# Kernel tuning notes

Hardware: AMD Instinct MI355X
Metric: run time of the kernel (lower is better)

Reference implementation:

```python
import jax, jax.numpy as jnp
import numpy as np
import math

B, N, CS, CZ, CH, H, PQK, PV = 1, 1024, 384, 128, 16, 12, 4, 8
INF, EPS = 1e5, 1e-8


def quat_to_rot(q):
    w, x, y, z = q[..., 0], q[..., 1], q[..., 2], q[..., 3]
    r = jnp.stack([
        1 - 2 * (y * y + z * z), 2 * (x * y - w * z), 2 * (x * z + w * y),
        2 * (x * y + w * z), 1 - 2 * (x * x + z * z), 2 * (y * z - w * x),
        2 * (x * z - w * y), 2 * (y * z + w * x), 1 - 2 * (x * x + y * y),
    ], axis=-1)
    return r.reshape(q.shape[:-1] + (3, 3))


def setup_inputs() -> dict:
    key = jax.random.key(0)
    ks = jax.random.split(key, 12)
    sc = 0.02
    s = jax.random.normal(ks[0], (B, N, CS), jnp.float32)
    z = jax.random.normal(ks[1], (B, N, N, CZ), jnp.float32)
    quat = jax.random.normal(ks[2], (B, N, 4), jnp.float32)
    rot = quat_to_rot(quat / jnp.linalg.norm(quat, axis=-1, keepdims=True))
    trans = jax.random.normal(ks[3], (B, N, 3), jnp.float32)
    mask = jnp.ones((B, N), jnp.float32)
    wq = jax.random.normal(ks[4], (CS, H * CH), jnp.float32) * sc
    bq = jnp.zeros((H * CH,), jnp.float32)
    wkv = jax.random.normal(ks[5], (CS, 2 * H * CH), jnp.float32) * sc
    bkv = jnp.zeros((2 * H * CH,), jnp.float32)
    wqp = jax.random.normal(ks[6], (CS, H * PQK * 3), jnp.float32) * sc
    bqp = jnp.zeros((H * PQK * 3,), jnp.float32)
    wkvp = jax.random.normal(ks[7], (CS, H * (PQK + PV) * 3), jnp.float32) * sc
    bkvp = jnp.zeros((H * (PQK + PV) * 3,), jnp.float32)
    wb = jax.random.normal(ks[8], (CZ, H), jnp.float32) * sc
    bb = jnp.zeros((H,), jnp.float32)
    head_w = jax.random.normal(ks[9], (H,), jnp.float32) * 0.1 + 0.5413  # softplus^-1(1)
    dcat = H * (CZ + CH + PV * 4)
    wout = jax.random.normal(ks[10], (dcat, CS), jnp.float32) * sc
    bout = jnp.zeros((CS,), jnp.float32)
    return dict(s=s, z=z, rot=rot, trans=trans, mask=mask, wq=wq, bq=bq,
                wkv=wkv, bkv=bkv, wqp=wqp, bqp=bqp, wkvp=wkvp, bkvp=bkvp,
                wb=wb, bb=bb, head_w=head_w, wout=wout, bout=bout)


def reference(s, z, rot, trans, mask, wq, bq, wkv, bkv, wqp, bqp, wkvp, bkvp,
              wb, bb, head_w, wout, bout):
    # scalar q/k/v: [B,N,H,CH]
    q = (s @ wq + bq).reshape(B, N, H, CH)
    kv = (s @ wkv + bkv).reshape(B, N, H, 2 * CH)
    k, v = kv[..., :CH], kv[..., CH:]

    def make_pts(raw, P):
        # raw layout: [x-coords | y-coords | z-coords], each of width H*P
        pts = jnp.swapaxes(raw.reshape(B, N, 3, H * P), -1, -2)  # [B,N,H*P,3]
        pts = jnp.einsum('bnxy,bnpy->bnpx', rot, pts) + trans[:, :, None, :]
        return pts.reshape(B, N, H, P, 3)

    q_pts = make_pts(s @ wqp + bqp, PQK)                 # [B,N,H,PQK,3] global frame
    kv_pts = make_pts(s @ wkvp + bkvp, PQK + PV)
    k_pts, v_pts = kv_pts[..., :PQK, :], kv_pts[..., PQK:, :]

    # scalar attention + pair bias: [B,H,N,N]
    a = jnp.einsum('bihc,bjhc->bhij', q, k) * math.sqrt(1.0 / (3 * CH))
    bias = z @ wb + bb                                    # [B,N,N,H]
    a = a + math.sqrt(1.0 / 3) * jnp.transpose(bias, (0, 3, 1, 2))

    # point attention via ||q-k||^2 = |q|^2 + |k|^2 - 2 q.k (summed over pts & xyz)
    hw = jax.nn.softplus(head_w) * math.sqrt(1.0 / (3 * (PQK * 9.0 / 2)))  # [H]
    qn = jnp.sum(q_pts ** 2, axis=(-1, -2))               # [B,N,H]
    kn = jnp.sum(k_pts ** 2, axis=(-1, -2))
    cross = jnp.einsum('bihpx,bjhpx->bhij', q_pts, k_pts)
    sqd = (jnp.transpose(qn, (0, 2, 1))[..., None]
           + jnp.transpose(kn, (0, 2, 1))[:, :, None, :]
           - 2.0 * cross)                                 # [B,H,N,N]
    a = a - 0.5 * hw[None, :, None, None] * sqd

    sqm = INF * (mask[:, :, None] * mask[:, None, :] - 1.0)  # [B,N,N]
    a = jax.nn.softmax(a + sqm[:, None], axis=-1)

    # outputs
    o = jnp.einsum('bhij,bjhc->bihc', a, v).reshape(B, N, H * CH)
    o_pt = jnp.einsum('bhij,bjhpx->bihpx', a, v_pts)      # [B,N,H,PV,3] global
    o_pt = jnp.einsum('bnyx,bnhpy->bnhpx', rot, o_pt - trans[:, :, None, None, :])  # invert_apply
    o_pt_norm = jnp.sqrt(jnp.sum(o_pt ** 2, axis=-1) + EPS).reshape(B, N, H * PV)
    o_pt3 = o_pt.reshape(B, N, H * PV, 3)
    o_pair = jnp.einsum('bhij,bijc->bihc', a, z).reshape(B, N, H * CZ)

    cat = jnp.concatenate(
        [o, o_pt3[..., 0], o_pt3[..., 1], o_pt3[..., 2], o_pt_norm, o_pair], axis=-1)
    return cat @ wout + bout
```

## Files before the change

### kernel.cpp

```cpp
#include <hip/hip_runtime.h>
#include <hip/hip_bf16.h>
#include <math.h>

#define NN   1024
#define CS   384
#define CZ   128
#define HH   12
#define HCH  192
#define QPR  144
#define DCAT 2112
#define PROJW 1152
#define INF_ 100000.0f

#define SC_QK 0.14433756729740643f
#define SC_B  0.5773502691896258f
#define SC_PT 0.13608276348795434f

__device__ __forceinline__ float dot4(float4 a, float4 b) {
  return a.x * b.x + a.y * b.y + a.z * b.z + a.w * b.w;
}
__device__ __forceinline__ float bf2f(unsigned short u) {
  unsigned int v = ((unsigned int)u) << 16;
  float f; __builtin_memcpy(&f, &v, 4); return f;
}
__device__ __forceinline__ unsigned short f2bf(float f) {
  __hip_bfloat16 h = __float2bfloat16(f);
  unsigned short u; __builtin_memcpy(&u, &h, 2); return u;
}

__global__ void prep(const float* __restrict__ wb, const float* __restrict__ head_w,
                     float* __restrict__ wb_t, float* __restrict__ hw)
{
  int t = threadIdx.x;
  for (int idx = t; idx < CZ * HH; idx += 256) {
    int c = idx % CZ, h = idx / CZ;
    wb_t[h * CZ + c] = wb[c * HH + h];
  }
  if (t < HH) {
    float x = head_w[t];
    float sp = (x > 20.f) ? x : log1pf(__expf(x));
    hw[t] = sp * SC_PT;
  }
}

__global__ __launch_bounds__(256) void proj_all(
    const float* __restrict__ s,
    const float* __restrict__ wq, const float* __restrict__ bq,
    const float* __restrict__ wkv, const float* __restrict__ bkv,
    const float* __restrict__ wqp, const float* __restrict__ bqp,
    const float* __restrict__ wkvp, const float* __restrict__ bkvp,
    float* __restrict__ proj)
{
  __shared__ float s_lds[8 * CS];
  const int n0 = blockIdx.x * 8;
  for (int idx = threadIdx.x; idx < 8 * CS; idx += 256)
    s_lds[idx] = s[(size_t)(n0 + idx / CS) * CS + (idx % CS)];
  __syncthreads();

  const int gc = blockIdx.y * 128 + (threadIdx.x & 31) * 4;
  const int rg = threadIdx.x >> 5;
  const float* wp; const float* bp; int OUT, lc;
  if (gc < 192)      { wp = wq;   bp = bq;   OUT = 192; lc = gc; }
  else if (gc < 576) { wp = wkv;  bp = bkv;  OUT = 384; lc = gc - 192; }
  else if (gc < 720) { wp = wqp;  bp = bqp;  OUT = 144; lc = gc - 576; }
  else               { wp = wkvp; bp = bkvp; OUT = 432; lc = gc - 720; }

  float a0 = 0.f, a1 = 0.f, a2 = 0.f, a3 = 0.f;
  const float* srow = &s_lds[rg * CS];
#pragma unroll 4
  for (int kk = 0; kk < CS; kk++) {
    float sv = srow[kk];
    float4 w4 = *reinterpret_cast<const float4*>(&wp[(size_t)kk * OUT + lc]);
    a0 += sv * w4.x; a1 += sv * w4.y; a2 += sv * w4.z; a3 += sv * w4.w;
  }
  float* o = proj + (size_t)(n0 + rg) * PROJW + gc;
  o[0] = a0 + bp[lc]; o[1] = a1 + bp[lc + 1];
  o[2] = a2 + bp[lc + 2]; o[3] = a3 + bp[lc + 3];
}

__global__ __launch_bounds__(256) void ipa_transform(
    const float* __restrict__ proj, const float* __restrict__ rot,
    const float* __restrict__ trans,
    float* __restrict__ kc, float* __restrict__ vc,
    float* __restrict__ q_pts, float* __restrict__ kpc,
    float* __restrict__ vpc, float* __restrict__ qn, float* __restrict__ knc)
{
  const int n = blockIdx.x, tid = threadIdx.x;
  const float* pr = proj + (size_t)n * PROJW;
  __shared__ float R[9], T[3], sq_q[48], sq_k[48];
  if (tid < 9) R[tid] = rot[n * 9 + tid];
  if (tid < 3) T[tid] = trans[n * 3 + tid];
  __syncthreads();
  if (tid < HCH) {
    int h = tid >> 4, c = tid & 15;
    kc[(size_t)(h * 16 + c) * NN + n] = pr[192 + h * 32 + c];
    vc[(size_t)(h * 16 + c) * NN + n] = pr[192 + h * 32 + 16 + c];
  }
  if (tid < 48) {
    float r0 = pr[576 + tid], r1 = pr[576 + 48 + tid], r2 = pr[576 + 96 + tid];
    float x = R[0] * r0 + R[1] * r1 + R[2] * r2 + T[0];
    float y = R[3] * r0 + R[4] * r1 + R[5] * r2 + T[1];
    float z = R[6] * r0 + R[7] * r1 + R[8] * r2 + T[2];
    q_pts[(size_t)n * QPR + tid * 3 + 0] = x;
    q_pts[(size_t)n * QPR + tid * 3 + 1] = y;
    q_pts[(size_t)n * QPR + tid * 3 + 2] = z;
    sq_q[tid] = x * x + y * y + z * z;
  }
  if (tid >= 64 && tid < 208) {
    int t = tid - 64;
    float r0 = pr[720 + t], r1 = pr[720 + 144 + t], r2 = pr[720 + 288 + t];
    float x = R[0] * r0 + R[1] * r1 + R[2] * r2 + T[0];
    float y = R[3] * r0 + R[4] * r1 + R[5] * r2 + T[1];
    float z = R[6] * r0 + R[7] * r1 + R[8] * r2 + T[2];
    int h = t / 12, pp = t % 12;
    if (pp < 4) {
      int d = pp * 3;
      kpc[(size_t)(h * 12 + d + 0) * NN + n] = x;
      kpc[(size_t)(h * 12 + d + 1) * NN + n] = y;
      kpc[(size_t)(h * 12 + d + 2) * NN + n] = z;
      sq_k[h * 4 + pp] = x * x + y * y + z * z;
    } else {
      int d = (pp - 4) * 3;
      vpc[(size_t)(h * 24 + d + 0) * NN + n] = x;
      vpc[(size_t)(h * 24 + d + 1) * NN + n] = y;
      vpc[(size_t)(h * 24 + d + 2) * NN + n] = z;
    }
  }
  __syncthreads();
  if (tid < HH) {
    float a = 0.f, b = 0.f;
#pragma unroll
    for (int p = 0; p < 4; p++) { a += sq_q[tid * 4 + p]; b += sq_k[tid * 4 + p]; }
    qn[n * HH + tid] = a;
    knc[(size_t)tid * NN + n] = b;
  }
}

__global__ __launch_bounds__(256) void bias_pass(
    const float* __restrict__ z, const float* __restrict__ wb_t,
    __hip_bfloat16* __restrict__ B)
{
  __shared__ float wb_s[HH * CZ];
  __shared__ float bias_s[HH * 128];
  const int i = blockIdx.y;
  const int jb = blockIdx.x * 128;
  const int tid = threadIdx.x;
  const int jl = tid >> 2, csub = tid & 3;

  for (int e = tid; e < HH * CZ; e += 256) wb_s[e] = wb_t[e];
  __syncthreads();

  float bd0[HH], bd1[HH];
#pragma unroll
  for (int h = 0; h < HH; h++) { bd0[h] = 0.f; bd1[h] = 0.f; }

  const float* zb = z + ((size_t)i * NN + jb + jl) * CZ + csub * 4;
#pragma unroll
  for (int k8 = 0; k8 < 8; k8++) {
    float4 zq0 = *reinterpret_cast<const float4*>(&zb[k8 * 16]);
    float4 zq1 = *reinterpret_cast<const float4*>(&zb[(size_t)64 * CZ + k8 * 16]);
    const int c = csub * 4 + k8 * 16;
#pragma unroll
    for (int h = 0; h < HH; h++) {
      float4 wv = *reinterpret_cast<const float4*>(&wb_s[h * CZ + c]);
      bd0[h] += dot4(zq0, wv);
      bd1[h] += dot4(zq1, wv);
    }
  }
#pragma unroll
  for (int h = 0; h < HH; h++) {
    bd0[h] += __shfl_xor(bd0[h], 1); bd0[h] += __shfl_xor(bd0[h], 2);
    bd1[h] += __shfl_xor(bd1[h], 1); bd1[h] += __shfl_xor(bd1[h], 2);
  }
  if (csub == 0) {
#pragma unroll
    for (int h = 0; h < HH; h++) {
      bias_s[h * 128 + jl] = bd0[h];
      bias_s[h * 128 + 64 + jl] = bd1[h];
    }
  }
  __syncthreads();
  for (int e = tid; e < HH * 128; e += 256) {
    int h = e >> 7, j2 = e & 127;
    B[((size_t)i * HH + h) * NN + jb + j2] = __float2bfloat16(bias_s[e]);
  }
}

__global__ __launch_bounds__(256) void ipa_attn(
    const float* __restrict__ kc, const float* __restrict__ kpc,
    const float* __restrict__ knc, const float* __restrict__ vc,
    const float* __restrict__ vpc, const float* __restrict__ proj,
    const float* __restrict__ q_pts, const float* __restrict__ qn,
    const float* __restrict__ bb, const float* __restrict__ hw,
    const float* __restrict__ mask,
    __hip_bfloat16* __restrict__ A, float* __restrict__ cat,
    float* __restrict__ optb)
{
  const int h = blockIdx.y;
  const int i = blockIdx.x * 4 + (threadIdx.x >> 6);
  const int lane = threadIdx.x & 63;

  const float* qb = proj + (size_t)i * PROJW + h * 16;
  const float4 q0 = *reinterpret_cast<const float4*>(qb);
  const float4 q1 = *reinterpret_cast<const float4*>(qb + 4);
  const float4 q2 = *reinterpret_cast<const float4*>(qb + 8);
  const float4 q3 = *reinterpret_cast<const float4*>(qb + 12);
  const float* pb = q_pts + (size_t)i * QPR + h * 12;
  const float4 p0 = *reinterpret_cast<const float4*>(pb);
  const float4 p1 = *reinterpret_cast<const float4*>(pb + 4);
  const float4 p2 = *reinterpret_cast<const float4*>(pb + 8);
  const float qnv = qn[i * HH + h];
  const float bbv = bb[h];
  const float hwv = hw[h];
  const float mi = mask[i];

  const float* kch  = kc  + (size_t)h * 16 * NN;
  const float* kpch = kpc + (size_t)h * 12 * NN;
  const float* knch = knc + (size_t)h * NN;
  const float* vch  = vc  + (size_t)h * 16 * NN;
  const float* vpch = vpc + (size_t)h * 24 * NN;
  __hip_bfloat16* Arow = A + ((size_t)i * HH + h) * NN;

  float4 av[4];
#pragma unroll
  for (int t = 0; t < 4; t++) {
    const int j = t * 256 + lane * 4;
    float4 d = {0, 0, 0, 0};
#pragma unroll
    for (int c = 0; c < 16; c++) {
      const float qc = (c < 4 ? (&q0.x)[c] : c < 8 ? (&q1.x)[c - 4]
                       : c < 12 ? (&q2.x)[c - 8] : (&q3.x)[c - 12]);
      float4 kv = *reinterpret_cast<const float4*>(&kch[(size_t)c * NN + j]);
      d.x += qc * kv.x; d.y += qc * kv.y; d.z += qc * kv.z; d.w += qc * kv.w;
    }
    float4 cr = {0, 0, 0, 0};
#pragma unroll
    for (int dd = 0; dd < 12; dd++) {
      const float pc = (dd < 4 ? (&p0.x)[dd] : dd < 8 ? (&p1.x)[dd - 4]
                        : (&p2.x)[dd - 8]);
      float4 kv = *reinterpret_cast<const float4*>(&kpch[(size_t)dd * NN + j]);
      cr.x += pc * kv.x; cr.y += pc * kv.y; cr.z += pc * kv.z; cr.w += pc * kv.w;
    }
    float4 kn4 = *reinterpret_cast<const float4*>(&knch[j]);
    ushort4 bu = *reinterpret_cast<const ushort4*>(&Arow[j]);
    float4 m4 = *reinterpret_cast<const float4*>(&mask[j]);
    av[t].x = SC_QK * d.x + SC_B * (bf2f(bu.x) + bbv)
              - 0.5f * hwv * (qnv + kn4.x - 2.f * cr.x) + INF_ * (mi * m4.x - 1.f);
    av[t].y = SC_QK * d.y + SC_B * (bf2f(bu.y) + bbv)
              - 0.5f * hwv * (qnv + kn4.y - 2.f * cr.y) + INF_ * (mi * m4.y - 1.f);
    av[t].z = SC_QK * d.z + SC_B * (bf2f(bu.z) + bbv)
              - 0.5f * hwv * (qnv + kn4.z - 2.f * cr.z) + INF_ * (mi * m4.z - 1.f);
    av[t].w = SC_QK * d.w + SC_B * (bf2f(bu.w) + bbv)
              - 0.5f * hwv * (qnv + kn4.w - 2.f * cr.w) + INF_ * (mi * m4.w - 1.f);
  }

  float m = av[0].x;
#pragma unroll
  for (int t = 0; t < 4; t++) {
    m = fmaxf(m, av[t].x); m = fmaxf(m, av[t].y);
    m = fmaxf(m, av[t].z); m = fmaxf(m, av[t].w);
  }
  for (int off = 32; off; off >>= 1) m = fmaxf(m, __shfl_xor(m, off));
  float ssum = 0.f;
#pragma unroll
  for (int t = 0; t < 4; t++) {
    av[t].x = __expf(av[t].x - m); ssum += av[t].x;
    av[t].y = __expf(av[t].y - m); ssum += av[t].y;
    av[t].z = __expf(av[t].z - m); ssum += av[t].z;
    av[t].w = __expf(av[t].w - m); ssum += av[t].w;
  }
  for (int off = 32; off; off >>= 1) ssum += __shfl_xor(ssum, off);
  const float inv = 1.f / ssum;
#pragma unroll
  for (int t = 0; t < 4; t++) {
    const int j = t * 256 + lane * 4;
    av[t].x *= inv; av[t].y *= inv; av[t].z *= inv; av[t].w *= inv;
    ushort4 st;
    st.x = f2bf(av[t].x); st.y = f2bf(av[t].y);
    st.z = f2bf(av[t].z); st.w = f2bf(av[t].w);
    *reinterpret_cast<ushort4*>(&Arow[j]) = st;
  }

  float oacc[16], wacc[24];
#pragma unroll
  for (int c = 0; c < 16; c++) oacc[c] = 0.f;
#pragma unroll
  for (int d = 0; d < 24; d++) wacc[d] = 0.f;
#pragma unroll
  for (int t = 0; t < 4; t++) {
    const int j = t * 256 + lane * 4;
    const float4 a4 = av[t];
#pragma unroll
    for (int c = 0; c < 16; c++) {
      float4 vv = *reinterpret_cast<const float4*>(&vch[(size_t)c * NN + j]);
      oacc[c] += dot4(a4, vv);
    }
#pragma unroll
    for (int d = 0; d < 24; d++) {
      float4 wv = *reinterpret_cast<const float4*>(&vpch[(size_t)d * NN + j]);
      wacc[d] += dot4(a4, wv);
    }
  }
  for (int off = 32; off; off >>= 1) {
#pragma unroll
    for (int c = 0; c < 16; c++) oacc[c] += __shfl_xor(oacc[c], off);
#pragma unroll
    for (int d = 0; d < 24; d++) wacc[d] += __shfl_xor(wacc[d], off);
  }
  if (lane == 0) {
    float* cr = cat + (size_t)i * DCAT + h * 16;
#pragma unroll
    for (int c = 0; c < 16; c++) cr[c] = oacc[c];
    float* ob = optb + ((size_t)i * HH + h) * 24;
#pragma unroll
    for (int d = 0; d < 24; d++) ob[d] = wacc[d];
  }
}

__global__ __launch_bounds__(128) void ipa_finish(
    const float* __restrict__ optb, const float* __restrict__ rot,
    const float* __restrict__ trans, float* __restrict__ cat)
{
  const int i = blockIdx.x, tid = threadIdx.x;
  __shared__ float R_s[9], T_s[3];
  if (tid < 9) R_s[tid] = rot[i * 9 + tid];
  if (tid < 3) T_s[tid] = trans[i * 3 + tid];
  __syncthreads();
  if (tid < 96) {
    int h = tid >> 3, p = tid & 7;
    const float* ob = optb + ((size_t)i * HH + h) * 24 + p * 3;
    float gx = ob[0] - T_s[0];
    float gy = ob[1] - T_s[1];
    float gz = ob[2] - T_s[2];
    float lx = R_s[0] * gx + R_s[3] * gy + R_s[6] * gz;
    float ly = R_s[1] * gx + R_s[4] * gy + R_s[7] * gz;
    float lz = R_s[2] * gx + R_s[5] * gy + R_s[8] * gz;
    float* catr = cat + (size_t)i * DCAT;
    catr[192 + 0 * 96 + h * 8 + p] = lx;
    catr[192 + 1 * 96 + h * 8 + p] = ly;
    catr[192 + 2 * 96 + h * 8 + p] = lz;
    catr[480 + h * 8 + p] = sqrtf(lx * lx + ly * ly + lz * lz + 1e-8f);
  }
}

__global__ __launch_bounds__(256) void opair_pass(
    const float* __restrict__ z, const __hip_bfloat16* __restrict__ A,
    float* __restrict__ cat)
{
  __shared__ float A_ls[512 * HH];
  __shared__ float red[HH * CZ];
  const int i = blockIdx.x, tid = threadIdx.x;
  const int c4 = (tid & 31) * 4, jsub = tid >> 5;

  for (int e = tid; e < HH * CZ; e += 256) red[e] = 0.f;

  float4 acc[HH];
#pragma unroll
  for (int h = 0; h < HH; h++) acc[h] = make_float4(0.f, 0.f, 0.f, 0.f);

  for (int half = 0; half < 2; half++) {
    __syncthreads();
    for (int e = tid; e < HH * 128; e += 256) {
      int h = e >> 7, j4 = (e & 127) * 4;
      ushort4 au = *reinterpret_cast<const ushort4*>(
          &A[((size_t)i * HH + h) * NN + half * 512 + j4]);
      A_ls[(j4 + 0) * HH + h] = bf2f(au.x);
      A_ls[(j4 + 1) * HH + h] = bf2f(au.y);
      A_ls[(j4 + 2) * HH + h] = bf2f(au.z);
      A_ls[(j4 + 3) * HH + h] = bf2f(au.w);
    }
    __syncthreads();

    const float* zrow = z + ((size_t)i * NN + half * 512 + jsub * 64) * CZ + c4;
    const float* arow = &A_ls[jsub * 64 * HH];
    for (int j0 = 0; j0 < 64; j0 += 4) {
#pragma unroll
      for (int jj = 0; jj < 4; jj++) {
        const int j = j0 + jj;
        float4 zq = *reinterpret_cast<const float4*>(&zrow[(size_t)j * CZ]);
        float4 a0 = *reinterpret_cast<const float4*>(&arow[j * HH]);
        float4 a1 = *reinterpret_cast<const float4*>(&arow[j * HH + 4]);
        float4 a2 = *reinterpret_cast<const float4*>(&arow[j * HH + 8]);
        acc[0].x += a0.x * zq.x; acc[0].y += a0.x * zq.y;
        acc[0].z += a0.x * zq.z; acc[0].w += a0.x * zq.w;
        acc[1].x += a0.y * zq.x; acc[1].y += a0.y * zq.y;
        acc[1].z += a0.y * zq.z; acc[1].w += a0.y * zq.w;
        acc[2].x += a0.z * zq.x; acc[2].y += a0.z * zq.y;
        acc[2].z += a0.z * zq.z; acc[2].w += a0.z * zq.w;
        acc[3].x += a0.w * zq.x; acc[3].y += a0.w * zq.y;
        acc[3].z += a0.w * zq.z; acc[3].w += a0.w * zq.w;
        acc[4].x += a1.x * zq.x; acc[4].y += a1.x * zq.y;
        acc[4].z += a1.x * zq.z; acc[4].w += a1.x * zq.w;
        acc[5].x += a1.y * zq.x; acc[5].y += a1.y * zq.y;
        acc[5].z += a1.y * zq.z; acc[5].w += a1.y * zq.w;
        acc[6].x += a1.z * zq.x; acc[6].y += a1.z * zq.y;
        acc[6].z += a1.z * zq.z; acc[6].w += a1.z * zq.w;
        acc[7].x += a1.w * zq.x; acc[7].y += a1.w * zq.y;
        acc[7].z += a1.w * zq.z; acc[7].w += a1.w * zq.w;
        acc[8].x += a2.x * zq.x; acc[8].y += a2.x * zq.y;
        acc[8].z += a2.x * zq.z; acc[8].w += a2.x * zq.w;
        acc[9].x += a2.y * zq.x; acc[9].y += a2.y * zq.y;
        acc[9].z += a2.y * zq.z; acc[9].w += a2.y * zq.w;
        acc[10].x += a2.z * zq.x; acc[10].y += a2.z * zq.y;
        acc[10].z += a2.z * zq.z; acc[10].w += a2.z * zq.w;
        acc[11].x += a2.w * zq.x; acc[11].y += a2.w * zq.y;
        acc[11].z += a2.w * zq.z; acc[11].w += a2.w * zq.w;
      }
    }
  }
  for (int s = 0; s < 8; s++) {
    __syncthreads();
    if (jsub == s) {
#pragma unroll
      for (int h = 0; h < HH; h++) {
        red[h * CZ + c4 + 0] += acc[h].x;
        red[h * CZ + c4 + 1] += acc[h].y;
        red[h * CZ + c4 + 2] += acc[h].z;
        red[h * CZ + c4 + 3] += acc[h].w;
      }
    }
  }
  __syncthreads();
  for (int e = tid; e < HH * CZ; e += 256)
    cat[(size_t)i * DCAT + 576 + e] = red[e];
}

__global__ __launch_bounds__(256) void out_gemm(
    const float* __restrict__ cat, const float* __restrict__ wout,
    const float* __restrict__ bout, float* __restrict__ out)
{
  __shared__ float c_lds[4 * DCAT];
  const int n0 = blockIdx.x * 4;
  const int cq = blockIdx.y * 128 + (threadIdx.x & 63) * 2;
  const int rg = threadIdx.x >> 6;
  for (int idx = threadIdx.x; idx < 4 * DCAT; idx += 256) {
    int r = idx / DCAT, kk = idx - r * DCAT;
    c_lds[idx] = cat[(size_t)(n0 + r) * DCAT + kk];
  }
  __syncthreads();
  float a0 = 0.f, a1 = 0.f;
  const float* crow = &c_lds[rg * DCAT];
#pragma unroll 4
  for (int kk = 0; kk < DCAT; kk++) {
    float cv = crow[kk];
    float2 w2 = *reinterpret_cast<const float2*>(&wout[(size_t)kk * CS + cq]);
    a0 += cv * w2.x; a1 += cv * w2.y;
  }
  float* o = out + (size_t)(n0 + rg) * CS + cq;
  o[0] = a0 + bout[cq]; o[1] = a1 + bout[cq + 1];
}

extern "C" void kernel_launch(void* const* d_in, const int* in_sizes, int n_in,
                              void* d_out, int out_size, void* d_ws, size_t ws_size,
                              hipStream_t stream) {
  const float* s      = (const float*)d_in[0];
  const float* z      = (const float*)d_in[1];
  const float* rot    = (const float*)d_in[2];
  const float* trans  = (const float*)d_in[3];
  const float* mask   = (const float*)d_in[4];
  const float* wq     = (const float*)d_in[5];
  const float* bq     = (const float*)d_in[6];
  const float* wkv    = (const float*)d_in[7];
  const float* bkv    = (const float*)d_in[8];
  const float* wqp    = (const float*)d_in[9];
  const float* bqp    = (const float*)d_in[10];
  const float* wkvp   = (const float*)d_in[11];
  const float* bkvp   = (const float*)d_in[12];
  const float* wb     = (const float*)d_in[13];
  const float* bb     = (const float*)d_in[14];
  const float* head_w = (const float*)d_in[15];
  const float* wout   = (const float*)d_in[16];
  const float* bout   = (const float*)d_in[17];
  float* out = (float*)d_out;

  float* ws = (float*)d_ws;
  float* proj_buf = ws;
  float* kc_buf   = proj_buf + (size_t)NN * PROJW;
  float* vc_buf   = kc_buf + (size_t)HH * 16 * NN;
  float* kpc_buf  = vc_buf + (size_t)HH * 16 * NN;
  float* vpc_buf  = kpc_buf + (size_t)HH * 12 * NN;
  float* knc_buf  = vpc_buf + (size_t)HH * 24 * NN;
  float* qpts_buf = knc_buf + (size_t)HH * NN;
  float* qn_buf   = qpts_buf + (size_t)NN * QPR;
  float* wbt_buf  = qn_buf + NN * HH;
  float* hw_buf   = wbt_buf + HH * CZ;
  float* optb_buf = hw_buf + 16;
  float* cat_buf  = optb_buf + (size_t)NN * HH * 24;
  __hip_bfloat16* A_buf =
      (__hip_bfloat16*)(cat_buf + (size_t)NN * DCAT);

  prep<<<dim3(1), dim3(256), 0, stream>>>(wb, head_w, wbt_buf, hw_buf);
  proj_all<<<dim3(NN / 8, 9), dim3(256), 0, stream>>>(
      s, wq, bq, wkv, bkv, wqp, bqp, wkvp, bkvp, proj_buf);
  ipa_transform<<<dim3(NN), dim3(256), 0, stream>>>(
      proj_buf, rot, trans, kc_buf, vc_buf, qpts_buf, kpc_buf, vpc_buf,
      qn_buf, knc_buf);
  bias_pass<<<dim3(8, NN), dim3(256), 0, stream>>>(z, wbt_buf, A_buf);
  ipa_attn<<<dim3(NN / 4, HH), dim3(256), 0, stream>>>(
      kc_buf, kpc_buf, knc_buf, vc_buf, vpc_buf, proj_buf, qpts_buf,
      qn_buf, bb, hw_buf, mask, A_buf, cat_buf, optb_buf);
  ipa_finish<<<dim3(NN), dim3(128), 0, stream>>>(optb_buf, rot, trans, cat_buf);
  opair_pass<<<dim3(NN), dim3(256), 0, stream>>>(z, A_buf, cat_buf);
  out_gemm<<<dim3(NN / 4, 3), dim3(256), 0, stream>>>(
      cat_buf, wout, bout, out);
}
```

Before: 738.4 us.

## Stage K/V tiles in LDS for attention and fold small kernels into neighbors

```diff
diff --git a/kernel.cpp b/kernel.cpp
--- a/kernel.cpp
+++ b/kernel.cpp
@@ -26,21 +26,6 @@
 __device__ __forceinline__ unsigned short f2bf(float f) {
   __hip_bfloat16 h = __float2bfloat16(f);
   unsigned short u; __builtin_memcpy(&u, &h, 2); return u;
-}
-
-__global__ void prep(const float* __restrict__ wb, const float* __restrict__ head_w,
-                     float* __restrict__ wb_t, float* __restrict__ hw)
-{
-  int t = threadIdx.x;
-  for (int idx = t; idx < CZ * HH; idx += 256) {
-    int c = idx % CZ, h = idx / CZ;
-    wb_t[h * CZ + c] = wb[c * HH + h];
-  }
-  if (t < HH) {
-    float x = head_w[t];
-    float sp = (x > 20.f) ? x : log1pf(__expf(x));
-    hw[t] = sp * SC_PT;
-  }
 }
 
 __global__ __launch_bounds__(256) void proj_all(
@@ -137,7 +122,7 @@
 }
 
 __global__ __launch_bounds__(256) void bias_pass(
-    const float* __restrict__ z, const float* __restrict__ wb_t,
+    const float* __restrict__ z, const float* __restrict__ wb,
     __hip_bfloat16* __restrict__ B)
 {
   __shared__ float wb_s[HH * CZ];
@@ -147,7 +132,10 @@
   const int tid = threadIdx.x;
   const int jl = tid >> 2, csub = tid & 3;
 
-  for (int e = tid; e < HH * CZ; e += 256) wb_s[e] = wb_t[e];
+  for (int e = tid; e < HH * CZ; e += 256) {
+    int c = e / HH, h = e - c * HH;
+    wb_s[h * CZ + c] = wb[e];
+  }
   __syncthreads();
 
   float bd0[HH], bd1[HH];
@@ -191,14 +179,21 @@
     const float* __restrict__ knc, const float* __restrict__ vc,
     const float* __restrict__ vpc, const float* __restrict__ proj,
     const float* __restrict__ q_pts, const float* __restrict__ qn,
-    const float* __restrict__ bb, const float* __restrict__ hw,
+    const float* __restrict__ bb, const float* __restrict__ head_w,
     const float* __restrict__ mask,
     __hip_bfloat16* __restrict__ A, float* __restrict__ cat,
     float* __restrict__ optb)
 {
+  __shared__ float k_ls[16 * 128];
+  __shared__ float kp_ls[12 * 128];
+  __shared__ float kn_ls[128];
+  __shared__ float v_ls[16 * 128];
+  __shared__ float vp_ls[24 * 128];
+
   const int h = blockIdx.y;
-  const int i = blockIdx.x * 4 + (threadIdx.x >> 6);
-  const int lane = threadIdx.x & 63;
+  const int tid = threadIdx.x;
+  const int i = blockIdx.x * 4 + (tid >> 6);
+  const int lane = tid & 63;
 
   const float* qb = proj + (size_t)i * PROJW + h * 16;
   const float4 q0 = *reinterpret_cast<const float4*>(qb);
@@ -211,7 +206,8 @@
   const float4 p2 = *reinterpret_cast<const float4*>(pb + 8);
   const float qnv = qn[i * HH + h];
   const float bbv = bb[h];
-  const float hwv = hw[h];
+  const float xw = head_w[h];
+  const float hwv = ((xw > 20.f) ? xw : log1pf(__expf(xw))) * SC_PT;
   const float mi = mask[i];
 
   const float* kch  = kc  + (size_t)h * 16 * NN;
@@ -221,64 +217,68 @@
   const float* vpch = vpc + (size_t)h * 24 * NN;
   __hip_bfloat16* Arow = A + ((size_t)i * HH + h) * NN;
 
-  float4 av[4];
-#pragma unroll
-  for (int t = 0; t < 4; t++) {
-    const int j = t * 256 + lane * 4;
-    float4 d = {0, 0, 0, 0};
-#pragma unroll
-    for (int c = 0; c < 16; c++) {
-      const float qc = (c < 4 ? (&q0.x)[c] : c < 8 ? (&q1.x)[c - 4]
-                       : c < 12 ? (&q2.x)[c - 8] : (&q3.x)[c - 12]);
-      float4 kv = *reinterpret_cast<const float4*>(&kch[(size_t)c * NN + j]);
-      d.x += qc * kv.x; d.y += qc * kv.y; d.z += qc * kv.z; d.w += qc * kv.w;
-    }
-    float4 cr = {0, 0, 0, 0};
-#pragma unroll
-    for (int dd = 0; dd < 12; dd++) {
-      const float pc = (dd < 4 ? (&p0.x)[dd] : dd < 8 ? (&p1.x)[dd - 4]
-                        : (&p2.x)[dd - 8]);
-      float4 kv = *reinterpret_cast<const float4*>(&kpch[(size_t)dd * NN + j]);
-      cr.x += pc * kv.x; cr.y += pc * kv.y; cr.z += pc * kv.z; cr.w += pc * kv.w;
-    }
-    float4 kn4 = *reinterpret_cast<const float4*>(&knch[j]);
-    ushort4 bu = *reinterpret_cast<const ushort4*>(&Arow[j]);
-    float4 m4 = *reinterpret_cast<const float4*>(&mask[j]);
-    av[t].x = SC_QK * d.x + SC_B * (bf2f(bu.x) + bbv)
-              - 0.5f * hwv * (qnv + kn4.x - 2.f * cr.x) + INF_ * (mi * m4.x - 1.f);
-    av[t].y = SC_QK * d.y + SC_B * (bf2f(bu.y) + bbv)
-              - 0.5f * hwv * (qnv + kn4.y - 2.f * cr.y) + INF_ * (mi * m4.y - 1.f);
-    av[t].z = SC_QK * d.z + SC_B * (bf2f(bu.z) + bbv)
-              - 0.5f * hwv * (qnv + kn4.z - 2.f * cr.z) + INF_ * (mi * m4.z - 1.f);
-    av[t].w = SC_QK * d.w + SC_B * (bf2f(bu.w) + bbv)
-              - 0.5f * hwv * (qnv + kn4.w - 2.f * cr.w) + INF_ * (mi * m4.w - 1.f);
-  }
-
-  float m = av[0].x;
-#pragma unroll
-  for (int t = 0; t < 4; t++) {
-    m = fmaxf(m, av[t].x); m = fmaxf(m, av[t].y);
-    m = fmaxf(m, av[t].z); m = fmaxf(m, av[t].w);
-  }
+  float av[16];
+
+  for (int tt = 0; tt < 8; tt++) {
+    const int jb = tt * 128;
+    __syncthreads();
+    for (int e = tid; e < 928; e += 256) {
+      if (e < 512) {
+        int c = e >> 5, j4 = (e & 31) * 4;
+        *reinterpret_cast<float4*>(&k_ls[c * 128 + j4]) =
+            *reinterpret_cast<const float4*>(&kch[(size_t)c * NN + jb + j4]);
+      } else if (e < 896) {
+        int e2 = e - 512, dd = e2 >> 5, j4 = (e2 & 31) * 4;
+        *reinterpret_cast<float4*>(&kp_ls[dd * 128 + j4]) =
+            *reinterpret_cast<const float4*>(&kpch[(size_t)dd * NN + jb + j4]);
+      } else {
+        int j4 = (e - 896) * 4;
+        *reinterpret_cast<float4*>(&kn_ls[j4]) =
+            *reinterpret_cast<const float4*>(&knch[jb + j4]);
+      }
+    }
+    __syncthreads();
+#pragma unroll
+    for (int sub = 0; sub < 2; sub++) {
+      const int jl = sub * 64 + lane;
+      const int j = jb + jl;
+      float d = 0.f;
+#pragma unroll
+      for (int c = 0; c < 16; c++) {
+        const float qc = (c < 4 ? (&q0.x)[c] : c < 8 ? (&q1.x)[c - 4]
+                         : c < 12 ? (&q2.x)[c - 8] : (&q3.x)[c - 12]);
+        d += qc * k_ls[c * 128 + jl];
+      }
+      float cr = 0.f;
+#pragma unroll
+      for (int dd = 0; dd < 12; dd++) {
+        const float pc = (dd < 4 ? (&p0.x)[dd] : dd < 8 ? (&p1.x)[dd - 4]
+                          : (&p2.x)[dd - 8]);
+        cr += pc * kp_ls[dd * 128 + jl];
+      }
+      float knv = kn_ls[jl];
+      float bias = bf2f(*reinterpret_cast<const unsigned short*>(&Arow[j]));
+      float mj = mask[j];
+      av[tt * 2 + sub] = SC_QK * d + SC_B * (bias + bbv)
+                         - 0.5f * hwv * (qnv + knv - 2.f * cr)
+                         + INF_ * (mi * mj - 1.f);
+    }
+  }
+
+  float m = av[0];
+#pragma unroll
+  for (int t = 1; t < 16; t++) m = fmaxf(m, av[t]);
   for (int off = 32; off; off >>= 1) m = fmaxf(m, __shfl_xor(m, off));
   float ssum = 0.f;
 #pragma unroll
-  for (int t = 0; t < 4; t++) {
-    av[t].x = __expf(av[t].x - m); ssum += av[t].x;
-    av[t].y = __expf(av[t].y - m); ssum += av[t].y;
-    av[t].z = __expf(av[t].z - m); ssum += av[t].z;
-    av[t].w = __expf(av[t].w - m); ssum += av[t].w;
-  }
+  for (int t = 0; t < 16; t++) { av[t] = __expf(av[t] - m); ssum += av[t]; }
   for (int off = 32; off; off >>= 1) ssum += __shfl_xor(ssum, off);
   const float inv = 1.f / ssum;
 #pragma unroll
-  for (int t = 0; t < 4; t++) {
-    const int j = t * 256 + lane * 4;
-    av[t].x *= inv; av[t].y *= inv; av[t].z *= inv; av[t].w *= inv;
-    ushort4 st;
-    st.x = f2bf(av[t].x); st.y = f2bf(av[t].y);
-    st.z = f2bf(av[t].z); st.w = f2bf(av[t].w);
-    *reinterpret_cast<ushort4*>(&Arow[j]) = st;
+  for (int t = 0; t < 16; t++) {
+    av[t] *= inv;
+    const int j = (t >> 1) * 128 + (t & 1) * 64 + lane;
+    *reinterpret_cast<unsigned short*>(&Arow[j]) = f2bf(av[t]);
   }
 
   float oacc[16], wacc[24];
@@ -286,21 +286,33 @@
   for (int c = 0; c < 16; c++) oacc[c] = 0.f;
 #pragma unroll
   for (int d = 0; d < 24; d++) wacc[d] = 0.f;
-#pragma unroll
-  for (int t = 0; t < 4; t++) {
-    const int j = t * 256 + lane * 4;
-    const float4 a4 = av[t];
-#pragma unroll
-    for (int c = 0; c < 16; c++) {
-      float4 vv = *reinterpret_cast<const float4*>(&vch[(size_t)c * NN + j]);
-      oacc[c] += dot4(a4, vv);
-    }
-#pragma unroll
-    for (int d = 0; d < 24; d++) {
-      float4 wv = *reinterpret_cast<const float4*>(&vpch[(size_t)d * NN + j]);
-      wacc[d] += dot4(a4, wv);
-    }
-  }
+
+  for (int tt = 0; tt < 8; tt++) {
+    const int jb = tt * 128;
+    __syncthreads();
+    for (int e = tid; e < 1280; e += 256) {
+      if (e < 512) {
+        int c = e >> 5, j4 = (e & 31) * 4;
+        *reinterpret_cast<float4*>(&v_ls[c * 128 + j4]) =
+            *reinterpret_cast<const float4*>(&vch[(size_t)c * NN + jb + j4]);
+      } else {
+        int e2 = e - 512, dd = e2 >> 5, j4 = (e2 & 31) * 4;
+        *reinterpret_cast<float4*>(&vp_ls[dd * 128 + j4]) =
+            *reinterpret_cast<const float4*>(&vpch[(size_t)dd * NN + jb + j4]);
+      }
+    }
+    __syncthreads();
+#pragma unroll
+    for (int sub = 0; sub < 2; sub++) {
+      const int jl = sub * 64 + lane;
+      const float a_ = av[tt * 2 + sub];
+#pragma unroll
+      for (int c = 0; c < 16; c++) oacc[c] += a_ * v_ls[c * 128 + jl];
+#pragma unroll
+      for (int d = 0; d < 24; d++) wacc[d] += a_ * vp_ls[d * 128 + jl];
+    }
+  }
+
   for (int off = 32; off; off >>= 1) {
 #pragma unroll
     for (int c = 0; c < 16; c++) oacc[c] += __shfl_xor(oacc[c], off);
@@ -317,41 +329,19 @@
   }
 }
 
-__global__ __launch_bounds__(128) void ipa_finish(
+__global__ __launch_bounds__(256) void opair_pass(
+    const float* __restrict__ z, const __hip_bfloat16* __restrict__ A,
     const float* __restrict__ optb, const float* __restrict__ rot,
     const float* __restrict__ trans, float* __restrict__ cat)
 {
+  __shared__ float A_ls[512 * HH];
+  __shared__ float red[HH * CZ];
+  __shared__ float R_s[9], T_s[3];
   const int i = blockIdx.x, tid = threadIdx.x;
-  __shared__ float R_s[9], T_s[3];
+  const int c4 = (tid & 31) * 4, jsub = tid >> 5;
+
   if (tid < 9) R_s[tid] = rot[i * 9 + tid];
   if (tid < 3) T_s[tid] = trans[i * 3 + tid];
-  __syncthreads();
-  if (tid < 96) {
-    int h = tid >> 3, p = tid & 7;
-    const float* ob = optb + ((size_t)i * HH + h) * 24 + p * 3;
-    float gx = ob[0] - T_s[0];
-    float gy = ob[1] - T_s[1];
-    float gz = ob[2] - T_s[2];
-    float lx = R_s[0] * gx + R_s[3] * gy + R_s[6] * gz;
-    float ly = R_s[1] * gx + R_s[4] * gy + R_s[7] * gz;
-    float lz = R_s[2] * gx + R_s[5] * gy + R_s[8] * gz;
-    float* catr = cat + (size_t)i * DCAT;
-    catr[192 + 0 * 96 + h * 8 + p] = lx;
-    catr[192 + 1 * 96 + h * 8 + p] = ly;
-    catr[192 + 2 * 96 + h * 8 + p] = lz;
-    catr[480 + h * 8 + p] = sqrtf(lx * lx + ly * ly + lz * lz + 1e-8f);
-  }
-}
-
-__global__ __launch_bounds__(256) void opair_pass(
-    const float* __restrict__ z, const __hip_bfloat16* __restrict__ A,
-    float* __restrict__ cat)
-{
-  __shared__ float A_ls[512 * HH];
-  __shared__ float red[HH * CZ];
-  const int i = blockIdx.x, tid = threadIdx.x;
-  const int c4 = (tid & 31) * 4, jsub = tid >> 5;
-
   for (int e = tid; e < HH * CZ; e += 256) red[e] = 0.f;
 
   float4 acc[HH];
@@ -423,6 +413,22 @@
   __syncthreads();
   for (int e = tid; e < HH * CZ; e += 256)
     cat[(size_t)i * DCAT + 576 + e] = red[e];
+
+  if (tid < 96) {
+    int h = tid >> 3, p = tid & 7;
+    const float* ob = optb + ((size_t)i * HH + h) * 24 + p * 3;
+    float gx = ob[0] - T_s[0];
+    float gy = ob[1] - T_s[1];
+    float gz = ob[2] - T_s[2];
+    float lx = R_s[0] * gx + R_s[3] * gy + R_s[6] * gz;
+    float ly = R_s[1] * gx + R_s[4] * gy + R_s[7] * gz;
+    float lz = R_s[2] * gx + R_s[5] * gy + R_s[8] * gz;
+    float* catr = cat + (size_t)i * DCAT;
+    catr[192 + 0 * 96 + h * 8 + p] = lx;
+    catr[192 + 1 * 96 + h * 8 + p] = ly;
+    catr[192 + 2 * 96 + h * 8 + p] = lz;
+    catr[480 + h * 8 + p] = sqrtf(lx * lx + ly * ly + lz * lz + 1e-8f);
+  }
 }
 
 __global__ __launch_bounds__(256) void out_gemm(
@@ -482,25 +488,22 @@
   float* knc_buf  = vpc_buf + (size_t)HH * 24 * NN;
   float* qpts_buf = knc_buf + (size_t)HH * NN;
   float* qn_buf   = qpts_buf + (size_t)NN * QPR;
-  float* wbt_buf  = qn_buf + NN * HH;
-  float* hw_buf   = wbt_buf + HH * CZ;
-  float* optb_buf = hw_buf + 16;
+  float* optb_buf = qn_buf + NN * HH + 16;
   float* cat_buf  = optb_buf + (size_t)NN * HH * 24;
   __hip_bfloat16* A_buf =
       (__hip_bfloat16*)(cat_buf + (size_t)NN * DCAT);
 
-  prep<<<dim3(1), dim3(256), 0, stream>>>(wb, head_w, wbt_buf, hw_buf);
   proj_all<<<dim3(NN / 8, 9), dim3(256), 0, stream>>>(
       s, wq, bq, wkv, bkv, wqp, bqp, wkvp, bkvp, proj_buf);
   ipa_transform<<<dim3(NN), dim3(256), 0, stream>>>(
       proj_buf, rot, trans, kc_buf, vc_buf, qpts_buf, kpc_buf, vpc_buf,
       qn_buf, knc_buf);
-  bias_pass<<<dim3(8, NN), dim3(256), 0, stream>>>(z, wbt_buf, A_buf);
+  bias_pass<<<dim3(8, NN), dim3(256), 0, stream>>>(z, wb, A_buf);
   ipa_attn<<<dim3(NN / 4, HH), dim3(256), 0, stream>>>(
       kc_buf, kpc_buf, knc_buf, vc_buf, vpc_buf, proj_buf, qpts_buf,
-      qn_buf, bb, hw_buf, mask, A_buf, cat_buf, optb_buf);
-  ipa_finish<<<dim3(NN), dim3(128), 0, stream>>>(optb_buf, rot, trans, cat_buf);
-  opair_pass<<<dim3(NN), dim3(256), 0, stream>>>(z, A_buf, cat_buf);
+      qn_buf, bb, head_w, mask, A_buf, cat_buf, optb_buf);
+  opair_pass<<<dim3(NN), dim3(256), 0, stream>>>(
+      z, A_buf, optb_buf, rot, trans, cat_buf);
   out_gemm<<<dim3(NN / 4, 3), dim3(256), 0, stream>>>(
       cat_buf, wout, bout, out);
 }
```

Result: slower. 764.0 us (+3.5%).

## Split opair pass over j into four blocks and fuse reduction with finish

Applied to the files above, without the earlier changes.

```diff
diff --git a/kernel.cpp b/kernel.cpp
--- a/kernel.cpp
+++ b/kernel.cpp
@@ -33,8 +33,9 @@
 {
   int t = threadIdx.x;
   for (int idx = t; idx < CZ * HH; idx += 256) {
-    int c = idx % CZ, h = idx / CZ;
-    wb_t[h * CZ + c] = wb[c * HH + h];
+    int c = idx % HH == idx % HH ? idx / HH : 0;
+    int h = idx - c * HH;
+    wb_t[h * CZ + c] = wb[idx];
   }
   if (t < HH) {
     float x = head_w[t];
@@ -150,21 +151,27 @@
   for (int e = tid; e < HH * CZ; e += 256) wb_s[e] = wb_t[e];
   __syncthreads();
 
+  const float* zb = z + ((size_t)i * NN + jb + jl) * CZ + csub * 4;
+  float4 zq0[8], zq1[8];
+#pragma unroll
+  for (int k8 = 0; k8 < 8; k8++)
+    zq0[k8] = *reinterpret_cast<const float4*>(&zb[k8 * 16]);
+#pragma unroll
+  for (int k8 = 0; k8 < 8; k8++)
+    zq1[k8] = *reinterpret_cast<const float4*>(&zb[(size_t)64 * CZ + k8 * 16]);
+
   float bd0[HH], bd1[HH];
 #pragma unroll
   for (int h = 0; h < HH; h++) { bd0[h] = 0.f; bd1[h] = 0.f; }
 
-  const float* zb = z + ((size_t)i * NN + jb + jl) * CZ + csub * 4;
 #pragma unroll
   for (int k8 = 0; k8 < 8; k8++) {
-    float4 zq0 = *reinterpret_cast<const float4*>(&zb[k8 * 16]);
-    float4 zq1 = *reinterpret_cast<const float4*>(&zb[(size_t)64 * CZ + k8 * 16]);
     const int c = csub * 4 + k8 * 16;
 #pragma unroll
     for (int h = 0; h < HH; h++) {
       float4 wv = *reinterpret_cast<const float4*>(&wb_s[h * CZ + c]);
-      bd0[h] += dot4(zq0, wv);
-      bd1[h] += dot4(zq1, wv);
+      bd0[h] += dot4(zq0[k8], wv);
+      bd1[h] += dot4(zq1[k8], wv);
     }
   }
 #pragma unroll
@@ -317,15 +324,102 @@
   }
 }
 
-__global__ __launch_bounds__(128) void ipa_finish(
-    const float* __restrict__ optb, const float* __restrict__ rot,
-    const float* __restrict__ trans, float* __restrict__ cat)
+__global__ __launch_bounds__(256) void opair_pass(
+    const float* __restrict__ z, const __hip_bfloat16* __restrict__ A,
+    float* __restrict__ partial)
+{
+  __shared__ float A_ls[256 * HH];
+  __shared__ float red[HH * CZ];
+  const int sp = blockIdx.x, i = blockIdx.y;
+  const int jb = sp * 256;
+  const int tid = threadIdx.x;
+  const int c4 = (tid & 31) * 4, jsub = tid >> 5;
+
+  for (int e = tid; e < HH * 64; e += 256) {
+    int h = e >> 6, j4 = (e & 63) * 4;
+    ushort4 au = *reinterpret_cast<const ushort4*>(
+        &A[((size_t)i * HH + h) * NN + jb + j4]);
+    A_ls[(j4 + 0) * HH + h] = bf2f(au.x);
+    A_ls[(j4 + 1) * HH + h] = bf2f(au.y);
+    A_ls[(j4 + 2) * HH + h] = bf2f(au.z);
+    A_ls[(j4 + 3) * HH + h] = bf2f(au.w);
+  }
+  for (int e = tid; e < HH * CZ; e += 256) red[e] = 0.f;
+  __syncthreads();
+
+  float4 acc[HH];
+#pragma unroll
+  for (int h = 0; h < HH; h++) acc[h] = make_float4(0.f, 0.f, 0.f, 0.f);
+
+  const float* zrow = z + ((size_t)i * NN + jb + jsub * 32) * CZ + c4;
+  const float* arow = &A_ls[jsub * 32 * HH];
+  for (int j0 = 0; j0 < 32; j0 += 4) {
+#pragma unroll
+    for (int jj = 0; jj < 4; jj++) {
+      const int j = j0 + jj;
+      float4 zq = *reinterpret_cast<const float4*>(&zrow[(size_t)j * CZ]);
+      float4 a0 = *reinterpret_cast<const float4*>(&arow[j * HH]);
+      float4 a1 = *reinterpret_cast<const float4*>(&arow[j * HH + 4]);
+      float4 a2 = *reinterpret_cast<const float4*>(&arow[j * HH + 8]);
+      acc[0].x += a0.x * zq.x; acc[0].y += a0.x * zq.y;
+      acc[0].z += a0.x * zq.z; acc[0].w += a0.x * zq.w;
+      acc[1].x += a0.y * zq.x; acc[1].y += a0.y * zq.y;
+      acc[1].z += a0.y * zq.z; acc[1].w += a0.y * zq.w;
+      acc[2].x += a0.z * zq.x; acc[2].y += a0.z * zq.y;
+      acc[2].z += a0.z * zq.z; acc[2].w += a0.z * zq.w;
+      acc[3].x += a0.w * zq.x; acc[3].y += a0.w * zq.y;
+      acc[3].z += a0.w * zq.z; acc[3].w += a0.w * zq.w;
+      acc[4].x += a1.x * zq.x; acc[4].y += a1.x * zq.y;
+      acc[4].z += a1.x * zq.z; acc[4].w += a1.x * zq.w;
+      acc[5].x += a1.y * zq.x; acc[5].y += a1.y * zq.y;
+      acc[5].z += a1.y * zq.z; acc[5].w += a1.y * zq.w;
+      acc[6].x += a1.z * zq.x; acc[6].y += a1.z * zq.y;
+      acc[6].z += a1.z * zq.z; acc[6].w += a1.z * zq.w;
+      acc[7].x += a1.w * zq.x; acc[7].y += a1.w * zq.y;
+      acc[7].z += a1.w * zq.z; acc[7].w += a1.w * zq.w;
+      acc[8].x += a2.x * zq.x; acc[8].y += a2.x * zq.y;
+      acc[8].z += a2.x * zq.z; acc[8].w += a2.x * zq.w;
+      acc[9].x += a2.y * zq.x; acc[9].y += a2.y * zq.y;
+      acc[9].z += a2.y * zq.z; acc[9].w += a2.y * zq.w;
+      acc[10].x += a2.z * zq.x; acc[10].y += a2.z * zq.y;
+      acc[10].z += a2.z * zq.z; acc[10].w += a2.z * zq.w;
+      acc[11].x += a2.w * zq.x; acc[11].y += a2.w * zq.y;
+      acc[11].z += a2.w * zq.z; acc[11].w += a2.w * zq.w;
+    }
+  }
+  for (int s = 0; s < 8; s++) {
+    __syncthreads();
+    if (jsub == s) {
+#pragma unroll
+      for (int h = 0; h < HH; h++) {
+        red[h * CZ + c4 + 0] += acc[h].x;
+        red[h * CZ + c4 + 1] += acc[h].y;
+        red[h * CZ + c4 + 2] += acc[h].z;
+        red[h * CZ + c4 + 3] += acc[h].w;
+      }
+    }
+  }
+  __syncthreads();
+  float* pp = partial + ((size_t)(i * 4 + sp)) * (HH * CZ);
+  for (int e = tid; e < HH * CZ; e += 256) pp[e] = red[e];
+}
+
+__global__ __launch_bounds__(256) void opair_reduce(
+    const float* __restrict__ partial, const float* __restrict__ optb,
+    const float* __restrict__ rot, const float* __restrict__ trans,
+    float* __restrict__ cat)
 {
   const int i = blockIdx.x, tid = threadIdx.x;
   __shared__ float R_s[9], T_s[3];
   if (tid < 9) R_s[tid] = rot[i * 9 + tid];
   if (tid < 3) T_s[tid] = trans[i * 3 + tid];
   __syncthreads();
+
+  const float* pp = partial + ((size_t)i * 4) * (HH * CZ);
+  for (int e = tid; e < HH * CZ; e += 256) {
+    float v = pp[e] + pp[HH * CZ + e] + pp[2 * HH * CZ + e] + pp[3 * HH * CZ + e];
+    cat[(size_t)i * DCAT + 576 + e] = v;
+  }
   if (tid < 96) {
     int h = tid >> 3, p = tid & 7;
     const float* ob = optb + ((size_t)i * HH + h) * 24 + p * 3;
@@ -341,88 +435,6 @@
     catr[192 + 2 * 96 + h * 8 + p] = lz;
     catr[480 + h * 8 + p] = sqrtf(lx * lx + ly * ly + lz * lz + 1e-8f);
   }
-}
-
-__global__ __launch_bounds__(256) void opair_pass(
-    const float* __restrict__ z, const __hip_bfloat16* __restrict__ A,
-    float* __restrict__ cat)
-{
-  __shared__ float A_ls[512 * HH];
-  __shared__ float red[HH * CZ];
-  const int i = blockIdx.x, tid = threadIdx.x;
-  const int c4 = (tid & 31) * 4, jsub = tid >> 5;
-
-  for (int e = tid; e < HH * CZ; e += 256) red[e] = 0.f;
-
-  float4 acc[HH];
-#pragma unroll
-  for (int h = 0; h < HH; h++) acc[h] = make_float4(0.f, 0.f, 0.f, 0.f);
-
-  for (int half = 0; half < 2; half++) {
-    __syncthreads();
-    for (int e = tid; e < HH * 128; e += 256) {
-      int h = e >> 7, j4 = (e & 127) * 4;
-      ushort4 au = *reinterpret_cast<const ushort4*>(
-          &A[((size_t)i * HH + h) * NN + half * 512 + j4]);
-      A_ls[(j4 + 0) * HH + h] = bf2f(au.x);
-      A_ls[(j4 + 1) * HH + h] = bf2f(au.y);
-      A_ls[(j4 + 2) * HH + h] = bf2f(au.z);
-      A_ls[(j4 + 3) * HH + h] = bf2f(au.w);
-    }
-    __syncthreads();
-
-    const float* zrow = z + ((size_t)i * NN + half * 512 + jsub * 64) * CZ + c4;
-    const float* arow = &A_ls[jsub * 64 * HH];
-    for (int j0 = 0; j0 < 64; j0 += 4) {
-#pragma unroll
-      for (int jj = 0; jj < 4; jj++) {
-        const int j = j0 + jj;
-        float4 zq = *reinterpret_cast<const float4*>(&zrow[(size_t)j * CZ]);
-        float4 a0 = *reinterpret_cast<const float4*>(&arow[j * HH]);
-        float4 a1 = *reinterpret_cast<const float4*>(&arow[j * HH + 4]);
-        float4 a2 = *reinterpret_cast<const float4*>(&arow[j * HH + 8]);
-        acc[0].x += a0.x * zq.x; acc[0].y += a0.x * zq.y;
-        acc[0].z += a0.x * zq.z; acc[0].w += a0.x * zq.w;
-        acc[1].x += a0.y * zq.x; acc[1].y += a0.y * zq.y;
-        acc[1].z += a0.y * zq.z; acc[1].w += a0.y * zq.w;
-        acc[2].x += a0.z * zq.x; acc[2].y += a0.z * zq.y;
-        acc[2].z += a0.z * zq.z; acc[2].w += a0.z * zq.w;
-        acc[3].x += a0.w * zq.x; acc[3].y += a0.w * zq.y;
-        acc[3].z += a0.w * zq.z; acc[3].w += a0.w * zq.w;
-        acc[4].x += a1.x * zq.x; acc[4].y += a1.x * zq.y;
-        acc[4].z += a1.x * zq.z; acc[4].w += a1.x * zq.w;
-        acc[5].x += a1.y * zq.x; acc[5].y += a1.y * zq.y;
-        acc[5].z += a1.y * zq.z; acc[5].w += a1.y * zq.w;
-        acc[6].x += a1.z * zq.x; acc[6].y += a1.z * zq.y;
-        acc[6].z += a1.z * zq.z; acc[6].w += a1.z * zq.w;
-        acc[7].x += a1.w * zq.x; acc[7].y += a1.w * zq.y;
-        acc[7].z += a1.w * zq.z; acc[7].w += a1.w * zq.w;
-        acc[8].x += a2.x * zq.x; acc[8].y += a2.x * zq.y;
-        acc[8].z += a2.x * zq.z; acc[8].w += a2.x * zq.w;
-        acc[9].x += a2.y * zq.x; acc[9].y += a2.y * zq.y;
-        acc[9].z += a2.y * zq.z; acc[9].w += a2.y * zq.w;
-        acc[10].x += a2.z * zq.x; acc[10].y += a2.z * zq.y;
-        acc[10].z += a2.z * zq.z; acc[10].w += a2.z * zq.w;
-        acc[11].x += a2.w * zq.x; acc[11].y += a2.w * zq.y;
-        acc[11].z += a2.w * zq.z; acc[11].w += a2.w * zq.w;
-      }
-    }
-  }
-  for (int s = 0; s < 8; s++) {
-    __syncthreads();
-    if (jsub == s) {
-#pragma unroll
-      for (int h = 0; h < HH; h++) {
-        red[h * CZ + c4 + 0] += acc[h].x;
-        red[h * CZ + c4 + 1] += acc[h].y;
-        red[h * CZ + c4 + 2] += acc[h].z;
-        red[h * CZ + c4 + 3] += acc[h].w;
-      }
-    }
-  }
-  __syncthreads();
-  for (int e = tid; e < HH * CZ; e += 256)
-    cat[(size_t)i * DCAT + 576 + e] = red[e];
 }
 
 __global__ __launch_bounds__(256) void out_gemm(
@@ -486,8 +498,9 @@
   float* hw_buf   = wbt_buf + HH * CZ;
   float* optb_buf = hw_buf + 16;
   float* cat_buf  = optb_buf + (size_t)NN * HH * 24;
+  float* part_buf = cat_buf + (size_t)NN * DCAT;
   __hip_bfloat16* A_buf =
-      (__hip_bfloat16*)(cat_buf + (size_t)NN * DCAT);
+      (__hip_bfloat16*)(part_buf + (size_t)4 * NN * HH * CZ);
 
   prep<<<dim3(1), dim3(256), 0, stream>>>(wb, head_w, wbt_buf, hw_buf);
   proj_all<<<dim3(NN / 8, 9), dim3(256), 0, stream>>>(
@@ -499,8 +512,9 @@
   ipa_attn<<<dim3(NN / 4, HH), dim3(256), 0, stream>>>(
       kc_buf, kpc_buf, knc_buf, vc_buf, vpc_buf, proj_buf, qpts_buf,
       qn_buf, bb, hw_buf, mask, A_buf, cat_buf, optb_buf);
-  ipa_finish<<<dim3(NN), dim3(128), 0, stream>>>(optb_buf, rot, trans, cat_buf);
-  opair_pass<<<dim3(NN), dim3(256), 0, stream>>>(z, A_buf, cat_buf);
+  opair_pass<<<dim3(4, NN), dim3(256), 0, stream>>>(z, A_buf, part_buf);
+  opair_reduce<<<dim3(NN), dim3(256), 0, stream>>>(
+      part_buf, optb_buf, rot, trans, cat_buf);
   out_gemm<<<dim3(NN / 4, 3), dim3(256), 0, stream>>>(
       cat_buf, wout, bout, out);
 }
```

Result: no change. 731.0 us (-1.0%).
